# Performance work log

Hardware: AMD Instinct MI355X
Metric: run time of the kernel (lower is better)

## Reference

```python
import jax, jax.numpy as jnp
import numpy as np

C = 512
H_HEADS = 8
CTX_D = 768
GEO_D = 512
FFN_D = 4 * C
EPS = 1e-5


def _layernorm(x, g, b):
    mu = jnp.mean(x, axis=-1, keepdims=True)
    var = jnp.mean((x - mu) ** 2, axis=-1, keepdims=True)
    return (x - mu) * jax.lax.rsqrt(var + EPS) * g + b


def _cross_attn(x, ctx, Wq, Wk, Wv, Wo, bo, h):
    # x: (B, N, C), ctx: (B, S, Dctx)
    b, n, _ = x.shape
    s = ctx.shape[1]
    inner = Wq.shape[1]
    d = inner // h
    q = (x @ Wq).reshape(b, n, h, d)
    k = (ctx @ Wk).reshape(b, s, h, d)
    v = (ctx @ Wv).reshape(b, s, h, d)
    sim = jnp.einsum('bihd,bjhd->bhij', q, k) * (d ** -0.5)
    attn = jax.nn.softmax(sim, axis=-1)
    out = jnp.einsum('bhij,bjhd->bihd', attn, v).reshape(b, n, inner)
    return out @ Wo + bo


def setup_inputs() -> dict:
    key = jax.random.key(0)
    ks = jax.random.split(key, 24)
    std = lambda fan_in: 1.0 / np.sqrt(fan_in)
    inp = {
        'x': jax.random.normal(ks[0], (4, C, 64, 64), jnp.float32),
        'context': jax.random.normal(ks[1], (4, 77, CTX_D), jnp.float32),
        'geometry_tokens': jax.random.normal(ks[2], (4, 256, GEO_D), jnp.float32),
        # layernorm params (norm1..norm4)
        'g1': jnp.ones((C,)), 'b1': jnp.zeros((C,)),
        'g2': jnp.ones((C,)), 'b2': jnp.zeros((C,)),
        'g3': jnp.ones((C,)), 'b3': jnp.zeros((C,)),
        'g4': jnp.ones((C,)), 'b4': jnp.zeros((C,)),
        # cross-attention (context) weights
        'cWq': jax.random.normal(ks[3], (C, C)) * std(C),
        'cWk': jax.random.normal(ks[4], (CTX_D, C)) * std(CTX_D),
        'cWv': jax.random.normal(ks[5], (CTX_D, C)) * std(CTX_D),
        'cWo': jax.random.normal(ks[6], (C, C)) * std(C),
        'cbo': jnp.zeros((C,)),
        # geometry-attention weights
        'gWq': jax.random.normal(ks[7], (C, C)) * std(C),
        'gWk': jax.random.normal(ks[8], (GEO_D, C)) * std(GEO_D),
        'gWv': jax.random.normal(ks[9], (GEO_D, C)) * std(GEO_D),
        'gWo': jax.random.normal(ks[10], (C, C)) * std(C),
        'gbo': jnp.zeros((C,)),
        # FFN weights
        'W1': jax.random.normal(ks[11], (C, FFN_D)) * std(C),
        'bf1': jnp.zeros((FFN_D,)),
        'W2': jax.random.normal(ks[12], (FFN_D, C)) * std(FFN_D),
        'bf2': jnp.zeros((C,)),
    }
    return inp


def reference(x, context, geometry_tokens,
              g1, b1, g2, b2, g3, b3, g4, b4,
              cWq, cWk, cWv, cWo, cbo,
              gWq, gWk, gWv, gWo, gbo,
              W1, bf1, W2, bf2):
    b, c, h, w = x.shape
    t = x.reshape(b, c, h * w).transpose(0, 2, 1)  # (B, N, C)
    # self_attn is called with context=None -> identity, so this is t + norm1(t)
    t = t + _layernorm(t, g1, b1)
    t = t + _cross_attn(_layernorm(t, g2, b2), context, cWq, cWk, cWv, cWo, cbo, H_HEADS)
    t = t + _cross_attn(_layernorm(t, g3, b3), geometry_tokens, gWq, gWk, gWv, gWo, gbo, H_HEADS)
    hdn = jax.nn.gelu(_layernorm(t, g4, b4) @ W1 + bf1, approximate=False)
    t = t + hdn @ W2 + bf2
    return t.transpose(0, 2, 1).reshape(b, c, h, w)
```

## Files before the change

### kernel.cpp

```cpp
#include <hip/hip_runtime.h>
#include <hip/hip_bf16.h>

using bf16 = __hip_bfloat16;
typedef __attribute__((ext_vector_type(8))) short short8;
typedef __attribute__((ext_vector_type(4))) short short4v;
typedef __attribute__((ext_vector_type(4))) float floatx4;

#define DEVFN __device__ __forceinline__

DEVFN float bf2f(bf16 v) { return __bfloat162float(v); }
DEVFN bf16 f2bf(float v) { return __float2bfloat16(v); }
DEVFN float us2f(unsigned short u) {
    union { unsigned int i; float f; } c; c.i = ((unsigned int)u) << 16; return c.f;
}
DEVFN unsigned short f2bfbits(float v) {
    union { bf16 h; unsigned short u; } c; c.h = f2bf(v); return c.u;
}
DEVFN float loadF(const void* p, size_t i, int isf) {
    return isf ? ((const float*)p)[i] : us2f(((const unsigned short*)p)[i]);
}
DEVFN void gl_lds16(const bf16* g, short* l) {
    __builtin_amdgcn_global_load_lds(
        (const __attribute__((address_space(1))) unsigned int*)g,
        (__attribute__((address_space(3))) unsigned int*)l, 16, 0, 0);
}
DEVFN float fast_gelu(float v) {
    float u = v * (0.7978845608028654f + 0.0356774081f * v * v);
    float e = __expf(2.f * u);
    float th = 1.f - 2.f / (e + 1.f);
    return 0.5f * v * (1.f + th);
}

__global__ __launch_bounds__(256) void detect_kernel(const void* x, int* flag)
{
    __shared__ int any;
    if (threadIdx.x == 0) any = 0;
    __syncthreads();
    const unsigned short* p = (const unsigned short*)x;
    int hit = 0;
    for (int i = threadIdx.x; i < 8192; i += 256) {
        if ((p[i] & 0x7F80u) == 0x7F80u) hit = 1;
    }
    if (hit) any = 1;
    __syncthreads();
    if (threadIdx.x == 0) flag[0] = any;
}

__global__ __launch_bounds__(256) void convert_kernel(
    const void* __restrict__ src, bf16* __restrict__ dst, const int* __restrict__ flag, int n)
{
    int isf = *flag;
    int i = blockIdx.x * 256 + threadIdx.x;
    if (i < n) dst[i] = f2bf(loadF(src, i, isf));
}

struct SegTab {
    const void* src[12];
    int off[12];
    int cnt[12];
};
__global__ __launch_bounds__(256) void param_convert_kernel(
    SegTab tab, bf16* __restrict__ dst, const int* __restrict__ flag)
{
    int isf = *flag;
    int s = blockIdx.x;
    const void* src = tab.src[s];
    int off = tab.off[s], cnt = tab.cnt[s];
    for (int i = threadIdx.x; i < cnt; i += 256)
        dst[off + i] = f2bf(loadF(src, i, isf));
}

__global__ __launch_bounds__(256) void ln_in_kernel(
    const void* __restrict__ x, float* __restrict__ t,
    const bf16* __restrict__ g, const bf16* __restrict__ bta,
    const int* __restrict__ flag, int NN)
{
    __shared__ float tile[16][516];
    int isf = *flag;
    int b = blockIdx.y;
    int n0 = blockIdx.x * 16;
    int tid = threadIdx.x;
    int nx = tid & 15, cy = tid >> 4;
#pragma unroll
    for (int p = 0; p < 32; p++) {
        int c = p * 16 + cy;
        tile[nx][c] = loadF(x, ((size_t)b * 512 + c) * NN + n0 + nx, isf);
    }
    __syncthreads();
    int w = tid >> 6, lane = tid & 63;
    for (int rr = 0; rr < 4; rr++) {
        int r = w * 4 + rr;
        float4 v0 = *(const float4*)&tile[r][lane * 8];
        float4 v1 = *(const float4*)&tile[r][lane * 8 + 4];
        float vals[8] = {v0.x, v0.y, v0.z, v0.w, v1.x, v1.y, v1.z, v1.w};
        float s = 0.f;
#pragma unroll
        for (int i = 0; i < 8; i++) s += vals[i];
#pragma unroll
        for (int off = 32; off; off >>= 1) s += __shfl_xor(s, off, 64);
        float mu = s * (1.f / 512.f);
        float sq = 0.f;
#pragma unroll
        for (int i = 0; i < 8; i++) { float d = vals[i] - mu; sq += d * d; }
#pragma unroll
        for (int off = 32; off; off >>= 1) sq += __shfl_xor(sq, off, 64);
        float rs = rsqrtf(sq * (1.f / 512.f) + 1e-5f);
        float out[8];
#pragma unroll
        for (int i = 0; i < 8; i++) {
            int c = lane * 8 + i;
            out[i] = vals[i] + (vals[i] - mu) * rs * bf2f(g[c]) + bf2f(bta[c]);
        }
        float* tp = t + ((size_t)b * NN + n0 + r) * 512 + lane * 8;
        *(float4*)tp = make_float4(out[0], out[1], out[2], out[3]);
        *(float4*)(tp + 4) = make_float4(out[4], out[5], out[6], out[7]);
    }
}

__global__ __launch_bounds__(256) void transpose_out_kernel(
    const float* __restrict__ t, void* __restrict__ o, const int* __restrict__ flag,
    int C, int NN)
{
    __shared__ float tile[32][33];
    int isf = *flag;
    int b = blockIdx.z;
    int n0 = blockIdx.x * 32, c0 = blockIdx.y * 32;
    int tx = threadIdx.x, ty = threadIdx.y;
#pragma unroll
    for (int i = 0; i < 4; i++)
        tile[ty + i * 8][tx] = t[((size_t)b * NN + n0 + ty + i * 8) * C + c0 + tx];
    __syncthreads();
#pragma unroll
    for (int i = 0; i < 4; i++) {
        size_t oi = ((size_t)b * C + c0 + ty + i * 8) * NN + n0 + tx;
        float val = tile[tx][ty + i * 8];
        if (isf) ((float*)o)[oi] = val;
        else ((bf16*)o)[oi] = f2bf(val);
    }
}

__global__ __launch_bounds__(256) void transpose_w_kernel(
    const void* __restrict__ Wm, bf16* __restrict__ WT, const int* __restrict__ flag,
    int K, int Nc)
{
    __shared__ float tile[32][33];
    int isf = *flag;
    int n0 = blockIdx.x * 32, k0 = blockIdx.y * 32;
    int tx = threadIdx.x, ty = threadIdx.y;
#pragma unroll
    for (int i = 0; i < 4; i++)
        tile[ty + i * 8][tx] = loadF(Wm, (size_t)(k0 + ty + i * 8) * Nc + n0 + tx, isf);
    __syncthreads();
#pragma unroll
    for (int i = 0; i < 4; i++)
        WT[(size_t)(n0 + ty + i * 8) * K + k0 + tx] = f2bf(tile[tx][ty + i * 8]);
}

__global__ __launch_bounds__(256) void ln_kernel(
    const float* __restrict__ t, const bf16* __restrict__ g, const bf16* __restrict__ bta,
    bf16* __restrict__ outp, int Mrows)
{
    int w = threadIdx.x >> 6, lane = threadIdx.x & 63;
    int row = blockIdx.x * 4 + w;
    if (row >= Mrows) return;
    const float* xr = t + (size_t)row * 512;
    float4 v0 = *(const float4*)(xr + lane * 8);
    float4 v1 = *(const float4*)(xr + lane * 8 + 4);
    float vals[8] = {v0.x, v0.y, v0.z, v0.w, v1.x, v1.y, v1.z, v1.w};
    float s = 0.f;
#pragma unroll
    for (int i = 0; i < 8; i++) s += vals[i];
#pragma unroll
    for (int off = 32; off; off >>= 1) s += __shfl_xor(s, off, 64);
    float mu = s * (1.f / 512.f);
    float sq = 0.f;
#pragma unroll
    for (int i = 0; i < 8; i++) { float d = vals[i] - mu; sq += d * d; }
#pragma unroll
    for (int off = 32; off; off >>= 1) sq += __shfl_xor(sq, off, 64);
    float rs = rsqrtf(sq * (1.f / 512.f) + 1e-5f);
#pragma unroll
    for (int i = 0; i < 8; i++) {
        int c = lane * 8 + i;
        float y = (vals[i] - mu) * rs * bf2f(g[c]) + bf2f(bta[c]);
        outp[(size_t)row * 512 + c] = f2bf(y);
    }
}

template <int MODE>
__global__ __launch_bounds__(256) void gemm64(
    const bf16* __restrict__ A, const bf16* __restrict__ WT,
    const bf16* __restrict__ bias, void* __restrict__ outp,
    int M, int K, int Nc)
{
    __shared__ short As[64 * 32];
    __shared__ short Bs[64 * 32];
    const int tid = threadIdx.x;
    const int m0 = blockIdx.y * 64;
    const int n0 = blockIdx.x * 64;
    const int w = tid >> 6;
    const int lane = tid & 63;
    const int lm = lane & 15;
    const int lq = lane >> 4;

    floatx4 acc[4];
#pragma unroll
    for (int nb = 0; nb < 4; nb++) acc[nb] = (floatx4){0.f, 0.f, 0.f, 0.f};

    const int srow = tid >> 2;
    const int scol = (tid & 3) << 3;
    const int agrow = m0 + srow;
    const bool aok = agrow < M;
    const bf16* Aptr = A + (size_t)agrow * K + scol;
    const bf16* Bptr = WT + (size_t)(n0 + srow) * K + scol;

    for (int k0 = 0; k0 < K; k0 += 32) {
        __syncthreads();
        int4 av = make_int4(0, 0, 0, 0);
        if (aok) av = *(const int4*)(Aptr + k0);
        *(int4*)(&As[srow * 32 + scol]) = av;
        *(int4*)(&Bs[srow * 32 + scol]) = *(const int4*)(Bptr + k0);
        __syncthreads();
        short8 a = *(const short8*)(&As[(w * 16 + lm) * 32 + lq * 8]);
#pragma unroll
        for (int nb = 0; nb < 4; nb++) {
            short8 b = *(const short8*)(&Bs[(nb * 16 + lm) * 32 + lq * 8]);
            acc[nb] = __builtin_amdgcn_mfma_f32_16x16x32_bf16(a, b, acc[nb], 0, 0, 0);
        }
    }

#pragma unroll
    for (int nb = 0; nb < 4; nb++) {
        int col = n0 + nb * 16 + lm;
        float bv = bias ? bf2f(bias[col]) : 0.f;
#pragma unroll
        for (int r = 0; r < 4; r++) {
            int row = m0 + w * 16 + lq * 4 + r;
            if (row < M) {
                float v = acc[nb][r] + bv;
                if (MODE == 1) v = fast_gelu(v);
                if (MODE == 2) {
                    ((float*)outp)[(size_t)row * Nc + col] += v;
                } else {
                    ((bf16*)outp)[(size_t)row * Nc + col] = f2bf(v);
                }
            }
        }
    }
}

template <int MODE>
__global__ __launch_bounds__(256) void gemm128(
    const bf16* __restrict__ A, const bf16* __restrict__ WT,
    const bf16* __restrict__ bias, void* __restrict__ outp,
    int K, int Nc)
{
    __shared__ short As[3 * 128 * 32];
    __shared__ short Bs[3 * 128 * 32];
    const int tid = threadIdx.x;
    const int m0 = blockIdx.y * 128;
    const int n0 = blockIdx.x * 128;
    const int w = tid >> 6, lane = tid & 63;
    const int lm = lane & 15, lq = lane >> 4;
    const int wy = w >> 1, wx = w & 1;

    floatx4 acc[4][4];
#pragma unroll
    for (int cb = 0; cb < 4; cb++)
#pragma unroll
        for (int rb = 0; rb < 4; rb++) acc[cb][rb] = (floatx4){0.f, 0.f, 0.f, 0.f};

    const int c0 = w * 2, c1 = w * 2 + 1;
    const int lr = lane >> 2;
    const int lk = (((lane & 3) ^ (lr & 3)) << 3);
    const bf16* gA0 = A + (size_t)(m0 + c0 * 16 + lr) * K + lk;
    const bf16* gA1 = A + (size_t)(m0 + c1 * 16 + lr) * K + lk;
    const bf16* gB0 = WT + (size_t)(n0 + c0 * 16 + lr) * K + lk;
    const bf16* gB1 = WT + (size_t)(n0 + c1 * 16 + lr) * K + lk;

    auto STAGE = [&](int d, int koff) {
        short* la = As + d * 4096;
        short* lb = Bs + d * 4096;
        gl_lds16(gA0 + koff, la + c0 * 512);
        gl_lds16(gA1 + koff, la + c1 * 512);
        gl_lds16(gB0 + koff, lb + c0 * 512);
        gl_lds16(gB1 + koff, lb + c1 * 512);
    };

    const int nt = K >> 5;
    STAGE(0, 0);
    STAGE(1, 32);
    asm volatile("s_waitcnt vmcnt(4)\n\ts_barrier" ::: "memory");

    const int fsw = ((lq ^ (lm & 3)) * 8);
    int cur = 0, stg = 2;
    for (int t = 0; t < nt; ++t) {
        if (t + 2 < nt) STAGE(stg, (t + 2) << 5);
        const short* cA = As + cur * 4096;
        const short* cB = Bs + cur * 4096;
        short8 wf[4], xf[4];
#pragma unroll
        for (int cb = 0; cb < 4; cb++)
            wf[cb] = *(const short8*)(&cB[(wx * 64 + cb * 16 + lm) * 32 + fsw]);
#pragma unroll
        for (int rb = 0; rb < 4; rb++)
            xf[rb] = *(const short8*)(&cA[(wy * 64 + rb * 16 + lm) * 32 + fsw]);
        __builtin_amdgcn_s_setprio(1);
#pragma unroll
        for (int cb = 0; cb < 4; cb++)
#pragma unroll
            for (int rb = 0; rb < 4; rb++)
                acc[cb][rb] = __builtin_amdgcn_mfma_f32_16x16x32_bf16(wf[cb], xf[rb], acc[cb][rb], 0, 0, 0);
        __builtin_amdgcn_s_setprio(0);
        if (t + 1 < nt) {
            if (t + 2 < nt) {
                asm volatile("s_waitcnt vmcnt(4) lgkmcnt(0)\n\ts_barrier" ::: "memory");
            } else {
                asm volatile("s_waitcnt vmcnt(0) lgkmcnt(0)\n\ts_barrier" ::: "memory");
            }
        }
        cur = (cur == 2) ? 0 : cur + 1;
        stg = (stg == 2) ? 0 : stg + 1;
    }
    __syncthreads();

    float4 bias4[4];
#pragma unroll
    for (int cb = 0; cb < 4; cb++) {
        if (bias) {
            const bf16* bp = bias + n0 + wx * 64 + cb * 16 + lq * 4;
            bias4[cb] = make_float4(bf2f(bp[0]), bf2f(bp[1]), bf2f(bp[2]), bf2f(bp[3]));
        } else {
            bias4[cb] = make_float4(0.f, 0.f, 0.f, 0.f);
        }
    }

    if (MODE == 2) {
        float* po = (float*)outp;
#pragma unroll
        for (int rb = 0; rb < 4; rb++) {
            size_t m = m0 + wy * 64 + rb * 16 + lm;
#pragma unroll
            for (int cb = 0; cb < 4; cb++) {
                float* p = po + m * Nc + n0 + wx * 64 + cb * 16 + lq * 4;
                float4 f = *(float4*)p;
                f.x += acc[cb][rb][0] + bias4[cb].x;
                f.y += acc[cb][rb][1] + bias4[cb].y;
                f.z += acc[cb][rb][2] + bias4[cb].z;
                f.w += acc[cb][rb][3] + bias4[cb].w;
                *(float4*)p = f;
            }
        }
    } else {
        unsigned short* stgb = (unsigned short*)&As[w * 1024];
        unsigned short* op = (unsigned short*)outp;
#pragma unroll
        for (int rb = 0; rb < 4; rb++) {
#pragma unroll
            for (int cb = 0; cb < 4; cb++) {
                short4v pk;
#pragma unroll
                for (int r = 0; r < 4; r++) {
                    float vv = acc[cb][rb][r] + ((const float*)&bias4[cb])[r];
                    if (MODE == 1) vv = fast_gelu(vv);
                    pk[r] = (short)f2bfbits(vv);
                }
                int chunk = (cb * 2 + (lq >> 1)) ^ (lm & 7);
                *(short4v*)(&stgb[lm * 64 + chunk * 8 + (lq & 1) * 4]) = pk;
            }
#pragma unroll
            for (int p = 0; p < 2; p++) {
                int row = p * 8 + (lane >> 3);
                int chunk = lane & 7;
                short8 ov = *(const short8*)(&stgb[row * 64 + ((chunk ^ (row & 7)) * 8)]);
                size_t m = m0 + wy * 64 + rb * 16 + row;
                *(short8*)(op + m * Nc + n0 + wx * 64 + chunk * 8) = ov;
            }
        }
    }
}

template <int SPAD, int SVALID>
__global__ __launch_bounds__(256) void attn_mfma_kernel(
    const bf16* __restrict__ q, const bf16* __restrict__ k, const bf16* __restrict__ v,
    bf16* __restrict__ o, int N)
{
    constexpr int MB = SPAD / 16;
    constexpr int KS = SPAD / 32;
    __shared__ unsigned short lds[SPAD * 64 + 64 * SPAD];
    unsigned short* Ks = lds;
    unsigned short* Vt = lds + SPAD * 64;
    unsigned short* Pw = lds;

    const int tid = threadIdx.x;
    const int b = blockIdx.x >> 3;
    const int h = blockIdx.x & 7;
    const int n0 = blockIdx.y * 64;
    const int w = tid >> 6, lane = tid & 63;
    const int lm = lane & 15, lq = lane >> 4;

    const unsigned short* kp = (const unsigned short*)k;
    const unsigned short* vp = (const unsigned short*)v;
    for (int idx = tid * 8; idx < SPAD * 64; idx += 2048) {
        int s = idx >> 6, d0 = idx & 63;
        short8 kv = {0, 0, 0, 0, 0, 0, 0, 0};
        short8 vv = {0, 0, 0, 0, 0, 0, 0, 0};
        if (s < SVALID) {
            size_t gb = ((size_t)(b * SVALID + s)) * 512 + h * 64 + d0;
            kv = *(const short8*)(kp + gb);
            vv = *(const short8*)(vp + gb);
        }
        int kc = (d0 >> 3) ^ (s & 7);
        *(short8*)(&Ks[s * 64 + kc * 8]) = kv;
        const unsigned short* vvp = (const unsigned short*)&vv;
#pragma unroll
        for (int i = 0; i < 8; i++) {
            int d = d0 + i;
            int sc = (s >> 3) ^ (d & 7);
            Vt[d * SPAD + sc * 8 + (s & 7)] = vvp[i];
        }
    }

    const int q0 = n0 + w * 16;
    const unsigned short* qp = (const unsigned short*)q;
    size_t qbase = ((size_t)(b * N + q0 + lm)) * 512 + h * 64 + lq * 8;
    short8 qf0 = *(const short8*)(qp + qbase);
    short8 qf1 = *(const short8*)(qp + qbase + 32);
    __syncthreads();

    floatx4 sacc[MB];
#pragma unroll
    for (int mb = 0; mb < MB; mb++) sacc[mb] = (floatx4){0.f, 0.f, 0.f, 0.f};
#pragma unroll
    for (int mb = 0; mb < MB; mb++) {
        int srow = mb * 16 + lm;
        short8 a0 = *(const short8*)(&Ks[srow * 64 + ((lq ^ (lm & 7)) * 8)]);
        short8 a1 = *(const short8*)(&Ks[srow * 64 + (((4 + lq) ^ (lm & 7)) * 8)]);
        sacc[mb] = __builtin_amdgcn_mfma_f32_16x16x32_bf16(a0, qf0, sacc[mb], 0, 0, 0);
        sacc[mb] = __builtin_amdgcn_mfma_f32_16x16x32_bf16(a1, qf1, sacc[mb], 0, 0, 0);
    }

    float mx = -1e30f;
#pragma unroll
    for (int mb = 0; mb < MB; mb++)
#pragma unroll
        for (int r = 0; r < 4; r++) {
            int s = mb * 16 + lq * 4 + r;
            if (s < SVALID) mx = fmaxf(mx, sacc[mb][r]);
        }
    mx = fmaxf(mx, __shfl_xor(mx, 16, 64));
    mx = fmaxf(mx, __shfl_xor(mx, 32, 64));
    mx *= 0.125f;
    float sum = 0.f;
#pragma unroll
    for (int mb = 0; mb < MB; mb++)
#pragma unroll
        for (int r = 0; r < 4; r++) {
            int s = mb * 16 + lq * 4 + r;
            float e = (s < SVALID) ? __expf(sacc[mb][r] * 0.125f - mx) : 0.f;
            sacc[mb][r] = e;
            sum += e;
        }
    sum += __shfl_xor(sum, 16, 64);
    sum += __shfl_xor(sum, 32, 64);
    float inv = 1.f / sum;

    __syncthreads();

    unsigned short* Pme = Pw + w * 16 * SPAD;
#pragma unroll
    for (int mb = 0; mb < MB; mb++) {
        short4v pk;
        pk[0] = (short)f2bfbits(sacc[mb][0] * inv);
        pk[1] = (short)f2bfbits(sacc[mb][1] * inv);
        pk[2] = (short)f2bfbits(sacc[mb][2] * inv);
        pk[3] = (short)f2bfbits(sacc[mb][3] * inv);
        int chunk = (mb * 2 + (lq >> 1)) ^ (lm & 7);
        *(short4v*)(&Pme[lm * SPAD + chunk * 8 + (lq & 1) * 4]) = pk;
    }

    floatx4 oacc[4];
#pragma unroll
    for (int mb2 = 0; mb2 < 4; mb2++) oacc[mb2] = (floatx4){0.f, 0.f, 0.f, 0.f};
    for (int ks = 0; ks < KS; ks++) {
        int sch = ((ks * 4 + lq) ^ (lm & 7)) * 8;
        short8 bfrag = *(const short8*)(&Pme[lm * SPAD + sch]);
#pragma unroll
        for (int mb2 = 0; mb2 < 4; mb2++) {
            int d = mb2 * 16 + lm;
            short8 afrag = *(const short8*)(&Vt[d * SPAD + sch]);
            oacc[mb2] = __builtin_amdgcn_mfma_f32_16x16x32_bf16(afrag, bfrag, oacc[mb2], 0, 0, 0);
        }
    }

#pragma unroll
    for (int mb2 = 0; mb2 < 4; mb2++) {
        short4v ok;
        ok[0] = (short)f2bfbits(oacc[mb2][0]);
        ok[1] = (short)f2bfbits(oacc[mb2][1]);
        ok[2] = (short)f2bfbits(oacc[mb2][2]);
        ok[3] = (short)f2bfbits(oacc[mb2][3]);
        int chunk = (mb2 * 2 + (lq >> 1)) ^ (lm & 7);
        *(short4v*)(&Pme[lm * 64 + chunk * 8 + (lq & 1) * 4]) = ok;
    }
    unsigned short* op = (unsigned short*)o;
#pragma unroll
    for (int p = 0; p < 2; p++) {
        int row = p * 8 + (lane >> 3);
        int chunk = lane & 7;
        short8 ov = *(const short8*)(&Pme[row * 64 + ((chunk ^ (row & 7)) * 8)]);
        *(short8*)(op + ((size_t)(b * N + n0 + w * 16 + row)) * 512 + h * 64 + chunk * 8) = ov;
    }
}

extern "C" void kernel_launch(void* const* d_in, const int* in_sizes, int n_in,
                              void* d_out, int out_size, void* d_ws, size_t ws_size,
                              hipStream_t stream)
{
    const void* x   = d_in[0];
    const void* ctx = d_in[1];
    const void* geo = d_in[2];
    const void* g1 = d_in[3];  const void* b1 = d_in[4];
    const void* g2 = d_in[5];  const void* b2 = d_in[6];
    const void* g3 = d_in[7];  const void* b3 = d_in[8];
    const void* g4 = d_in[9];  const void* b4 = d_in[10];
    const void* cWq = d_in[11]; const void* cWk = d_in[12];
    const void* cWv = d_in[13]; const void* cWo = d_in[14];
    const void* cbo = d_in[15];
    const void* gWq = d_in[16]; const void* gWk = d_in[17];
    const void* gWv = d_in[18]; const void* gWo = d_in[19];
    const void* gbo = d_in[20];
    const void* W1 = d_in[21];  const void* bf1 = d_in[22];
    const void* W2 = d_in[23];  const void* bf2 = d_in[24];

    const int B = 4, C = 512, NN = 4096;
    const int M = B * NN;

    char* ws = (char*)d_ws;
    size_t off = 0;
    auto alloc = [&](size_t bytes) -> void* {
        void* p = ws + off; off += (bytes + 255) & ~(size_t)255; return p;
    };
    int*   flag = (int*)alloc(256);
    float* t  = (float*)alloc((size_t)M * C * 4);
    bf16* u   = (bf16*)alloc((size_t)M * C * 2);
    bf16* qb  = (bf16*)alloc((size_t)M * C * 2);
    bf16* kb  = (bf16*)alloc((size_t)B * 256 * C * 2);
    bf16* vb  = (bf16*)alloc((size_t)B * 256 * C * 2);
    bf16* ctxb = (bf16*)alloc((size_t)B * 77 * 768 * 2);
    bf16* geob = (bf16*)alloc((size_t)B * 256 * 512 * 2);
    bf16* cWqT = (bf16*)alloc((size_t)512 * 512 * 2);
    bf16* cWkT = (bf16*)alloc((size_t)512 * 768 * 2);
    bf16* cWvT = (bf16*)alloc((size_t)512 * 768 * 2);
    bf16* cWoT = (bf16*)alloc((size_t)512 * 512 * 2);
    bf16* gWqT = (bf16*)alloc((size_t)512 * 512 * 2);
    bf16* gWkT = (bf16*)alloc((size_t)512 * 512 * 2);
    bf16* gWvT = (bf16*)alloc((size_t)512 * 512 * 2);
    bf16* gWoT = (bf16*)alloc((size_t)512 * 512 * 2);
    bf16* W1T  = (bf16*)alloc((size_t)2048 * 512 * 2);
    bf16* W2T  = (bf16*)alloc((size_t)512 * 2048 * 2);
    bf16* prm  = (bf16*)alloc((size_t)7680 * 2);
    bf16* ob = u;

    int chunk;
    bf16* hb;
    size_t rem = (ws_size > off) ? (ws_size - off) : 0;
    if (rem >= (size_t)16384 * 2048 * 2) { chunk = 16384; hb = (bf16*)alloc((size_t)16384 * 2048 * 2); }
    else if (rem >= (size_t)8192 * 2048 * 2) { chunk = 8192; hb = (bf16*)alloc((size_t)8192 * 2048 * 2); }
    else { chunk = 4096; hb = qb; }
    (void)in_sizes; (void)n_in; (void)out_size;

    bf16 *pg1 = prm, *pb1 = prm + 512, *pg2 = prm + 1024, *pb2 = prm + 1536;
    bf16 *pg3 = prm + 2048, *pb3 = prm + 2560, *pg4 = prm + 3072, *pb4 = prm + 3584;
    bf16 *pcbo = prm + 4096, *pgbo = prm + 4608, *pbf1 = prm + 5120, *pbf2 = prm + 7168;

    dim3 tb(32, 8);

    detect_kernel<<<1, 256, 0, stream>>>(x, flag);
    SegTab tab;
    const void* srcs[12] = {g1, b1, g2, b2, g3, b3, g4, b4, cbo, gbo, bf1, bf2};
    int offs[12] = {0, 512, 1024, 1536, 2048, 2560, 3072, 3584, 4096, 4608, 5120, 7168};
    int cnts[12] = {512, 512, 512, 512, 512, 512, 512, 512, 512, 512, 2048, 512};
    for (int i = 0; i < 12; i++) { tab.src[i] = srcs[i]; tab.off[i] = offs[i]; tab.cnt[i] = cnts[i]; }
    param_convert_kernel<<<12, 256, 0, stream>>>(tab, prm, flag);
    convert_kernel<<<(B * 77 * 768 + 255) / 256, 256, 0, stream>>>(ctx, ctxb, flag, B * 77 * 768);
    convert_kernel<<<(B * 256 * 512 + 255) / 256, 256, 0, stream>>>(geo, geob, flag, B * 256 * 512);

    ln_in_kernel<<<dim3(NN / 16, B), 256, 0, stream>>>(x, t, pg1, pb1, flag, NN);

    transpose_w_kernel<<<dim3(512 / 32, 512 / 32), tb, 0, stream>>>(cWq, cWqT, flag, 512, 512);
    transpose_w_kernel<<<dim3(512 / 32, 768 / 32), tb, 0, stream>>>(cWk, cWkT, flag, 768, 512);
    transpose_w_kernel<<<dim3(512 / 32, 768 / 32), tb, 0, stream>>>(cWv, cWvT, flag, 768, 512);
    transpose_w_kernel<<<dim3(512 / 32, 512 / 32), tb, 0, stream>>>(cWo, cWoT, flag, 512, 512);
    transpose_w_kernel<<<dim3(512 / 32, 512 / 32), tb, 0, stream>>>(gWq, gWqT, flag, 512, 512);
    transpose_w_kernel<<<dim3(512 / 32, 512 / 32), tb, 0, stream>>>(gWk, gWkT, flag, 512, 512);
    transpose_w_kernel<<<dim3(512 / 32, 512 / 32), tb, 0, stream>>>(gWv, gWvT, flag, 512, 512);
    transpose_w_kernel<<<dim3(512 / 32, 512 / 32), tb, 0, stream>>>(gWo, gWoT, flag, 512, 512);
    transpose_w_kernel<<<dim3(2048 / 32, 512 / 32), tb, 0, stream>>>(W1, W1T, flag, 512, 2048);
    transpose_w_kernel<<<dim3(512 / 32, 2048 / 32), tb, 0, stream>>>(W2, W2T, flag, 2048, 512);

    ln_kernel<<<M / 4, 256, 0, stream>>>(t, pg2, pb2, u, M);
    gemm128<0><<<dim3(4, M / 128), 256, 0, stream>>>(u, cWqT, nullptr, qb, 512, 512);
    gemm64<0><<<dim3(8, (308 + 63) / 64), 256, 0, stream>>>(ctxb, cWkT, nullptr, kb, 308, 768, 512);
    gemm64<0><<<dim3(8, (308 + 63) / 64), 256, 0, stream>>>(ctxb, cWvT, nullptr, vb, 308, 768, 512);
    attn_mfma_kernel<128, 77><<<dim3(B * 8, NN / 64), 256, 0, stream>>>(qb, kb, vb, ob, NN);
    gemm128<2><<<dim3(4, M / 128), 256, 0, stream>>>(ob, cWoT, pcbo, t, 512, 512);

    ln_kernel<<<M / 4, 256, 0, stream>>>(t, pg3, pb3, u, M);
    gemm128<0><<<dim3(4, M / 128), 256, 0, stream>>>(u, gWqT, nullptr, qb, 512, 512);
    gemm64<0><<<dim3(8, 1024 / 64), 256, 0, stream>>>(geob, gWkT, nullptr, kb, 1024, 512, 512);
    gemm64<0><<<dim3(8, 1024 / 64), 256, 0, stream>>>(geob, gWvT, nullptr, vb, 1024, 512, 512);
    attn_mfma_kernel<256, 256><<<dim3(B * 8, NN / 64), 256, 0, stream>>>(qb, kb, vb, ob, NN);
    gemm128<2><<<dim3(4, M / 128), 256, 0, stream>>>(ob, gWoT, pgbo, t, 512, 512);

    ln_kernel<<<M / 4, 256, 0, stream>>>(t, pg4, pb4, u, M);
    for (int mc = 0; mc < M / chunk; mc++) {
        bf16* uc = u + (size_t)mc * chunk * 512;
        float* tc = t + (size_t)mc * chunk * 512;
        gemm128<1><<<dim3(2048 / 128, chunk / 128), 256, 0, stream>>>(uc, W1T, pbf1, hb, 512, 2048);
        gemm128<2><<<dim3(512 / 128, chunk / 128), 256, 0, stream>>>(hb, W2T, pbf2, tc, 2048, 512);
    }

    transpose_out_kernel<<<dim3(NN / 32, C / 32, B), tb, 0, stream>>>(t, d_out, flag, C, NN);
}
```

Baseline: 537.0 us.

## Enlarge GEMM tile to 256x128 with XCD-aware block swizzle

Replaces the 128x128 GEMM kernel with a 256x128 variant. Each warp now computes 128x64 outputs, which doubles A-tile reuse per loaded B fragment and halves the number of blocks. The LDS staging layout and the XOR swizzle are reworked to match the new tile. Block indices are remapped so that consecutive blocks land on the same XCD, aiming for better L2 locality. The cost is more accumulator registers (128 floats per lane) and larger LDS use, which can lower occupancy and leave fewer blocks per GPU for the smaller GEMMs.

```diff
diff --git a/kernel.cpp b/kernel.cpp
--- a/kernel.cpp
+++ b/kernel.cpp
@@ -250,71 +250,77 @@
 }
 
 template <int MODE>
-__global__ __launch_bounds__(256) void gemm128(
+__global__ __launch_bounds__(256, 2) void gemm256(
     const bf16* __restrict__ A, const bf16* __restrict__ WT,
     const bf16* __restrict__ bias, void* __restrict__ outp,
     int K, int Nc)
 {
-    __shared__ short As[3 * 128 * 32];
+    __shared__ short As[3 * 256 * 32];
     __shared__ short Bs[3 * 128 * 32];
     const int tid = threadIdx.x;
-    const int m0 = blockIdx.y * 128;
-    const int n0 = blockIdx.x * 128;
+
+    const int gx = gridDim.x;
+    int g = blockIdx.y * gx + blockIdx.x;
+    const int cpx = (gx * gridDim.y) >> 3;
+    g = (g & 7) * cpx + (g >> 3);
+    const int m0 = (g / gx) * 256;
+    const int n0 = (g % gx) * 128;
+
     const int w = tid >> 6, lane = tid & 63;
     const int lm = lane & 15, lq = lane >> 4;
     const int wy = w >> 1, wx = w & 1;
 
-    floatx4 acc[4][4];
+    floatx4 acc[4][8];
 #pragma unroll
     for (int cb = 0; cb < 4; cb++)
 #pragma unroll
-        for (int rb = 0; rb < 4; rb++) acc[cb][rb] = (floatx4){0.f, 0.f, 0.f, 0.f};
-
-    const int c0 = w * 2, c1 = w * 2 + 1;
+        for (int rb = 0; rb < 8; rb++) acc[cb][rb] = (floatx4){0.f, 0.f, 0.f, 0.f};
+
     const int lr = lane >> 2;
-    const int lk = (((lane & 3) ^ (lr & 3)) << 3);
-    const bf16* gA0 = A + (size_t)(m0 + c0 * 16 + lr) * K + lk;
-    const bf16* gA1 = A + (size_t)(m0 + c1 * 16 + lr) * K + lk;
-    const bf16* gB0 = WT + (size_t)(n0 + c0 * 16 + lr) * K + lk;
-    const bf16* gB1 = WT + (size_t)(n0 + c1 * 16 + lr) * K + lk;
+    const int lk = (((lane & 3) ^ ((lr >> 1) & 3)) << 3);
+    const bf16* gA = A + (size_t)(m0 + w * 64 + lr) * K + lk;
+    const bf16* gB = WT + (size_t)(n0 + w * 32 + lr) * K + lk;
+    const size_t K16 = (size_t)K * 16;
 
     auto STAGE = [&](int d, int koff) {
-        short* la = As + d * 4096;
-        short* lb = Bs + d * 4096;
-        gl_lds16(gA0 + koff, la + c0 * 512);
-        gl_lds16(gA1 + koff, la + c1 * 512);
-        gl_lds16(gB0 + koff, lb + c0 * 512);
-        gl_lds16(gB1 + koff, lb + c1 * 512);
+        short* la = As + d * 8192 + w * 2048;
+        short* lb = Bs + d * 4096 + w * 1024;
+        gl_lds16(gA + koff, la);
+        gl_lds16(gA + K16 + koff, la + 512);
+        gl_lds16(gA + 2 * K16 + koff, la + 1024);
+        gl_lds16(gA + 3 * K16 + koff, la + 1536);
+        gl_lds16(gB + koff, lb);
+        gl_lds16(gB + K16 + koff, lb + 512);
     };
 
     const int nt = K >> 5;
     STAGE(0, 0);
     STAGE(1, 32);
-    asm volatile("s_waitcnt vmcnt(4)\n\ts_barrier" ::: "memory");
-
-    const int fsw = ((lq ^ (lm & 3)) * 8);
+    asm volatile("s_waitcnt vmcnt(6)\n\ts_barrier" ::: "memory");
+
+    const int fsw = ((lq ^ ((lm >> 1) & 3)) * 8);
     int cur = 0, stg = 2;
     for (int t = 0; t < nt; ++t) {
         if (t + 2 < nt) STAGE(stg, (t + 2) << 5);
-        const short* cA = As + cur * 4096;
+        const short* cA = As + cur * 8192;
         const short* cB = Bs + cur * 4096;
-        short8 wf[4], xf[4];
+        short8 wf[4], xf[8];
 #pragma unroll
         for (int cb = 0; cb < 4; cb++)
             wf[cb] = *(const short8*)(&cB[(wx * 64 + cb * 16 + lm) * 32 + fsw]);
 #pragma unroll
-        for (int rb = 0; rb < 4; rb++)
-            xf[rb] = *(const short8*)(&cA[(wy * 64 + rb * 16 + lm) * 32 + fsw]);
+        for (int rb = 0; rb < 8; rb++)
+            xf[rb] = *(const short8*)(&cA[(wy * 128 + rb * 16 + lm) * 32 + fsw]);
         __builtin_amdgcn_s_setprio(1);
 #pragma unroll
         for (int cb = 0; cb < 4; cb++)
 #pragma unroll
-            for (int rb = 0; rb < 4; rb++)
+            for (int rb = 0; rb < 8; rb++)
                 acc[cb][rb] = __builtin_amdgcn_mfma_f32_16x16x32_bf16(wf[cb], xf[rb], acc[cb][rb], 0, 0, 0);
         __builtin_amdgcn_s_setprio(0);
         if (t + 1 < nt) {
             if (t + 2 < nt) {
-                asm volatile("s_waitcnt vmcnt(4) lgkmcnt(0)\n\ts_barrier" ::: "memory");
+                asm volatile("s_waitcnt vmcnt(6) lgkmcnt(0)\n\ts_barrier" ::: "memory");
             } else {
                 asm volatile("s_waitcnt vmcnt(0) lgkmcnt(0)\n\ts_barrier" ::: "memory");
             }
@@ -338,8 +344,8 @@
     if (MODE == 2) {
         float* po = (float*)outp;
 #pragma unroll
-        for (int rb = 0; rb < 4; rb++) {
-            size_t m = m0 + wy * 64 + rb * 16 + lm;
+        for (int rb = 0; rb < 8; rb++) {
+            size_t m = m0 + wy * 128 + rb * 16 + lm;
 #pragma unroll
             for (int cb = 0; cb < 4; cb++) {
                 float* p = po + m * Nc + n0 + wx * 64 + cb * 16 + lq * 4;
@@ -355,7 +361,7 @@
         unsigned short* stgb = (unsigned short*)&As[w * 1024];
         unsigned short* op = (unsigned short*)outp;
 #pragma unroll
-        for (int rb = 0; rb < 4; rb++) {
+        for (int rb = 0; rb < 8; rb++) {
 #pragma unroll
             for (int cb = 0; cb < 4; cb++) {
                 short4v pk;
@@ -373,7 +379,7 @@
                 int row = p * 8 + (lane >> 3);
                 int chunk = lane & 7;
                 short8 ov = *(const short8*)(&stgb[row * 64 + ((chunk ^ (row & 7)) * 8)]);
-                size_t m = m0 + wy * 64 + rb * 16 + row;
+                size_t m = m0 + wy * 128 + rb * 16 + row;
                 *(short8*)(op + m * Nc + n0 + wx * 64 + chunk * 8) = ov;
             }
         }
@@ -600,25 +606,25 @@
     transpose_w_kernel<<<dim3(512 / 32, 2048 / 32), tb, 0, stream>>>(W2, W2T, flag, 2048, 512);
 
     ln_kernel<<<M / 4, 256, 0, stream>>>(t, pg2, pb2, u, M);
-    gemm128<0><<<dim3(4, M / 128), 256, 0, stream>>>(u, cWqT, nullptr, qb, 512, 512);
+    gemm256<0><<<dim3(4, M / 256), 256, 0, stream>>>(u, cWqT, nullptr, qb, 512, 512);
     gemm64<0><<<dim3(8, (308 + 63) / 64), 256, 0, stream>>>(ctxb, cWkT, nullptr, kb, 308, 768, 512);
     gemm64<0><<<dim3(8, (308 + 63) / 64), 256, 0, stream>>>(ctxb, cWvT, nullptr, vb, 308, 768, 512);
     attn_mfma_kernel<128, 77><<<dim3(B * 8, NN / 64), 256, 0, stream>>>(qb, kb, vb, ob, NN);
-    gemm128<2><<<dim3(4, M / 128), 256, 0, stream>>>(ob, cWoT, pcbo, t, 512, 512);
+    gemm256<2><<<dim3(4, M / 256), 256, 0, stream>>>(ob, cWoT, pcbo, t, 512, 512);
 
     ln_kernel<<<M / 4, 256, 0, stream>>>(t, pg3, pb3, u, M);
-    gemm128<0><<<dim3(4, M / 128), 256, 0, stream>>>(u, gWqT, nullptr, qb, 512, 512);
+    gemm256<0><<<dim3(4, M / 256), 256, 0, stream>>>(u, gWqT, nullptr, qb, 512, 512);
     gemm64<0><<<dim3(8, 1024 / 64), 256, 0, stream>>>(geob, gWkT, nullptr, kb, 1024, 512, 512);
     gemm64<0><<<dim3(8, 1024 / 64), 256, 0, stream>>>(geob, gWvT, nullptr, vb, 1024, 512, 512);
     attn_mfma_kernel<256, 256><<<dim3(B * 8, NN / 64), 256, 0, stream>>>(qb, kb, vb, ob, NN);
-    gemm128<2><<<dim3(4, M / 128), 256, 0, stream>>>(ob, gWoT, pgbo, t, 512, 512);
+    gemm256<2><<<dim3(4, M / 256), 256, 0, stream>>>(ob, gWoT, pgbo, t, 512, 512);
 
     ln_kernel<<<M / 4, 256, 0, stream>>>(t, pg4, pb4, u, M);
     for (int mc = 0; mc < M / chunk; mc++) {
         bf16* uc = u + (size_t)mc * chunk * 512;
         float* tc = t + (size_t)mc * chunk * 512;
-        gemm128<1><<<dim3(2048 / 128, chunk / 128), 256, 0, stream>>>(uc, W1T, pbf1, hb, 512, 2048);
-        gemm128<2><<<dim3(512 / 128, chunk / 128), 256, 0, stream>>>(hb, W2T, pbf2, tc, 2048, 512);
+        gemm256<1><<<dim3(2048 / 128, chunk / 256), 256, 0, stream>>>(uc, W1T, pbf1, hb, 512, 2048);
+        gemm256<2><<<dim3(512 / 128, chunk / 256), 256, 0, stream>>>(hb, W2T, pbf2, tc, 2048, 512);
     }
 
     transpose_out_kernel<<<dim3(NN / 32, C / 32, B), tb, 0, stream>>>(t, d_out, flag, C, NN);
```

Measured after the change: 557.5 us. 3.8% more time.
